# Performance work log

Measured on AMD Instinct MI355X. Metric: run time of the kernel, lower is better.

The kernel has to match this reference:

```python
import jax, jax.numpy as jnp
import numpy as np

V, E, H, L, F, NQ, C = 32000, 256, 8, 4, 1024, 256, 10
B, S = 8, 1024
DK = E // H


def setup_inputs() -> dict:
    key = jax.random.key(0)
    ks = jax.random.split(key, 10)
    f = lambda k, shape, s=0.02: jax.random.normal(k, shape, jnp.float32) * s
    return {
        'tokens': jax.random.randint(ks[0], (B, S), 0, V, jnp.int32),
        'emb': f(ks[1], (V, E), 1.0),
        'theta_attn': f(ks[2], (L, H, DK), 0.5),
        'Wc': f(ks[3], (L, E, E)),
        'bc': jnp.zeros((L, E), jnp.float32),
        'g1': jnp.ones((L, E), jnp.float32),
        'bn1': jnp.zeros((L, E), jnp.float32),
        'theta_ffn': f(ks[4], (L, NQ), 0.5),
        'W1': f(ks[5], (L, NQ, F)),
        'b1': jnp.zeros((L, F), jnp.float32),
        'W2': f(ks[6], (L, F, E)),
        'b2': jnp.zeros((L, E), jnp.float32),
        'g2': jnp.ones((L, E), jnp.float32),
        'bn2': jnp.zeros((L, E), jnp.float32),
        'Wcls': f(ks[7], (E, C)),
        'bcls': jnp.zeros((C,), jnp.float32),
    }


def _ln(x, g, b, eps=1e-5):
    m = x.mean(-1, keepdims=True)
    v = ((x - m) ** 2).mean(-1, keepdims=True)
    return (x - m) / jnp.sqrt(v + eps) * g + b


def _pos_encoding(seq, dim):
    pos = jnp.arange(seq, dtype=jnp.float32)[:, None]
    div = jnp.exp(jnp.arange(0, dim, 2, dtype=jnp.float32) * (-np.log(10000.0) / dim))
    pe = jnp.zeros((seq, dim), jnp.float32)
    pe = pe.at[:, 0::2].set(jnp.sin(pos * div)).at[:, 1::2].set(jnp.cos(pos * div))
    return pe


def _qattn_proj(xh, theta):
    # xh: [B,S,H,dk], theta: [H,dk]. Circuit RX(x+th) per wire, CNOT ring, <Z_i>.
    # Analytic: <Z_i> = prod_{j<=i} cos(phi_j) for i>=1; <Z_0> = prod_{j>=1} cos(phi_j)
    c = jnp.cos(xh + theta)              # [B,S,H,dk]
    cum = jnp.cumprod(c, axis=-1)        # cum[...,i] = prod_{j<=i} c_j
    head0 = jnp.prod(c[..., 1:], axis=-1, keepdims=True)
    return jnp.concatenate([head0, cum[..., 1:]], axis=-1)  # [B,S,H,dk]


def _forward(tokens, emb, theta_attn, Wc, bc, g1, bn1, theta_ffn, W1, b1, W2, b2, g2, bn2, Wcls, bcls):
    b, s = tokens.shape
    x = emb[tokens] + _pos_encoding(s, E)  # [B,S,E]
    scale = 1.0 / np.sqrt(DK)
    for l in range(L):
        # quantum multi-head projection; q = k = v (same deterministic circuit)
        xh = x.reshape(b, s, H, DK)
        p = _qattn_proj(xh, theta_attn[l]).reshape(b, s, E)
        scores = jax.nn.softmax(jnp.einsum('bqe,bke->bqk', p, p) * scale, axis=-1)
        attn = jnp.einsum('bqk,bke->bqe', scores, p) @ Wc[l] + bc[l]
        x = _ln(x + attn, g1[l], bn1[l])
        # quantum FFN: <Z_i> = cos(x_i) * cos(theta_i), NQ == E here
        q = jnp.cos(x[..., :NQ]) * jnp.cos(theta_ffn[l])
        f = jax.nn.relu(q @ W1[l] + b1[l]) @ W2[l] + b2[l]
        x = _ln(x + f, g2[l], bn2[l])
    return x.mean(axis=1) @ Wcls + bcls  # [B,C]


def reference(tokens, emb, theta_attn, Wc, bc, g1, bn1, theta_ffn, W1, b1, W2, b2, g2, bn2, Wcls, bcls):
    return _forward(tokens, emb, theta_attn, Wc, bc, g1, bn1, theta_ffn, W1, b1, W2, b2, g2, bn2, Wcls, bcls)
```

## Files before the change

kernel.cpp:

```cpp
#include <hip/hip_runtime.h>
#include <hip/hip_bf16.h>
#include <math.h>

#define BB 8
#define SS 1024
#define EE 256
#define HH 8
#define DKK 32
#define LL 4
#define FF 1024
#define NQQ 256
#define CC 10

typedef __attribute__((ext_vector_type(8))) short short8;
typedef __attribute__((ext_vector_type(4))) short s16x4;
typedef __attribute__((ext_vector_type(4))) float f32x4;

static __device__ __forceinline__ f32x4 mfma16(short8 a, short8 b, f32x4 c) {
    return __builtin_amdgcn_mfma_f32_16x16x32_bf16(a, b, c, 0, 0, 0);
}
static __device__ __forceinline__ short f2bf(float f) {
    __hip_bfloat16 h = __float2bfloat16(f);
    return *reinterpret_cast<short*>(&h);
}

#define FRAG(P, tile, KG, kg, l) ((P) + (((size_t)((tile)*(KG) + (kg)))*64 + (l))*8)

static __device__ __forceinline__ void qproj_row(
        const float* __restrict__ xrow,
        const float* __restrict__ th,
        int b, int s, int h,
        short* __restrict__ PQ, short* __restrict__ PT) {
    float v[DKK];
    float cum = __cosf(xrow[h * DKK + 0] + th[0]);
    float prod1 = 1.0f;
    #pragma unroll
    for (int j = 1; j < DKK; ++j) {
        float c = __cosf(xrow[h * DKK + j] + th[j]);
        cum *= c;
        prod1 *= c;
        v[j] = cum;
    }
    v[0] = prod1;
    short* pq = PQ + (size_t)b * SS * EE;
    int stile = s >> 4, lr = s & 15;
    #pragma unroll
    for (int lg = 0; lg < 4; ++lg) {
        short8 u;
        #pragma unroll
        for (int j = 0; j < 8; ++j) u[j] = f2bf(v[lg*8 + j]);
        *(short8*)FRAG(pq, stile*8 + h, 1, 0, lg*16 + lr) = u;
    }
    short* pt = PT + (size_t)b * SS * EE;
    int kt = s >> 5, lgs = (s >> 3) & 3, j0 = s & 7;
    #pragma unroll
    for (int j = 0; j < DKK; ++j) {
        int e = h * DKK + j;
        FRAG(pt, e >> 4, 32, kt, lgs*16 + (e & 15))[j0] = f2bf(v[j]);
    }
}

__global__ __launch_bounds__(512) void k_embedq(
        const int* __restrict__ tokens, const float* __restrict__ emb,
        const float* __restrict__ theta_q,
        float* __restrict__ x, short* __restrict__ PQ, short* __restrict__ PT) {
    const int t = threadIdx.x;
    const int tok0 = blockIdx.x * 32;
    __shared__ float xls[32 * 268];
    {
        int r = t >> 4, c0 = (t & 15) * 16;
        int bs = tok0 + r;
        int s  = bs & (SS - 1);
        int tok = tokens[bs];
        const float* er = emb + (size_t)tok * EE + c0;
        float vals[16];
        #pragma unroll
        for (int i = 0; i < 16; ++i) {
            int col = c0 + i;
            int i2 = col >> 1;
            float div = __expf(-(float)(2 * i2) * (logf(10000.0f) / (float)EE));
            float ang = (float)s * div;
            float pe = (col & 1) ? __cosf(ang) : __sinf(ang);
            vals[i] = er[i] + pe;
            xls[r * 268 + col] = vals[i];
        }
        float* xg = x + (size_t)bs * EE + c0;
        #pragma unroll
        for (int i4 = 0; i4 < 4; ++i4)
            *(float4*)(xg + i4 * 4) = *(const float4*)&vals[i4 * 4];
    }
    __syncthreads();
    if (t < 256) {
        int sl = t >> 3, h = t & 7;
        int bs = tok0 + sl;
        qproj_row(&xls[sl * 268], theta_q + h * DKK,
                  bs >> 10, bs & (SS - 1), h, PQ, PT);
    }
}

__global__ __launch_bounds__(256) void k_trall(
        const float* __restrict__ W1, const float* __restrict__ W2,
        const float* __restrict__ Wc,
        short* __restrict__ W1P, short* __restrict__ W2P, short* __restrict__ WcP) {
    int bid = blockIdx.x;
    int lyr = bid / 576, rem = bid % 576;
    const float* in; short* out; int R, C, tile;
    if (rem < 256)      { in = W1 + (size_t)lyr*NQQ*FF; out = W1P + (size_t)lyr*FF*NQQ; R = NQQ; C = FF;  tile = rem; }
    else if (rem < 512) { in = W2 + (size_t)lyr*FF*EE;  out = W2P + (size_t)lyr*EE*FF;  R = FF;  C = EE;  tile = rem - 256; }
    else                { in = Wc + (size_t)lyr*EE*EE;  out = WcP + (size_t)lyr*EE*EE;  R = EE;  C = EE;  tile = rem - 512; }
    const int KG = R >> 5;
    int tiles_c = C >> 5;
    int tc = tile % tiles_c, tr = tile / tiles_c;
    __shared__ float tl[32][33];
    int t = threadIdx.x;
    int rr = t >> 5, cc = t & 31;
    #pragma unroll
    for (int i = 0; i < 4; ++i)
        tl[rr + i*8][cc] = in[(size_t)(tr*32 + rr + i*8) * C + tc*32 + cc];
    __syncthreads();
    int ro = t >> 3, co = (t & 7) * 4;
    int n = tc*32 + ro;
    int k = tr*32 + co;
    int ntile = n >> 4, lr = n & 15;
    int kg = k >> 5, lg = (k & 31) >> 3, j0 = k & 7;
    s16x4 v;
    v[0] = f2bf(tl[co + 0][ro]);
    v[1] = f2bf(tl[co + 1][ro]);
    v[2] = f2bf(tl[co + 2][ro]);
    v[3] = f2bf(tl[co + 3][ro]);
    *(s16x4*)(FRAG(out, ntile, KG, kg, lg*16 + lr) + j0) = v;
}

__global__ __launch_bounds__(256) void k_attn7(const short* __restrict__ PQ,
                                               const short* __restrict__ PT,
                                               short* __restrict__ YP) {
    const int b   = blockIdx.x >> 6;
    const int qt  = blockIdx.x & 63;
    const int tid = threadIdx.x;
    const int w   = tid >> 6;
    const int l   = tid & 63;
    const int lr  = l & 15, lg = l >> 4;
    const short* pq = PQ + (size_t)b * SS * EE;
    const short* pt = PT + (size_t)b * SS * EE;

    __shared__ float accP[2][16][264];
    __shared__ float lsL[4][16];
    __shared__ short wlds[4][16 * 40];

    short8 qf[8];
    #pragma unroll
    for (int kg = 0; kg < 8; ++kg)
        qf[kg] = *(const short8*)FRAG(pq, qt*8 + kg, 1, 0, l);

    f32x4 acc[16];
    #pragma unroll
    for (int i = 0; i < 16; ++i) acc[i] = f32x4{0.f, 0.f, 0.f, 0.f};
    float ls[4] = {0.f, 0.f, 0.f, 0.f};
    const float scale = 0.17677669529663687f;
    short* wl = wlds[w];

    for (int i = 0; i < 8; ++i) {
        const int kt = w + 4 * i;
        short8 sb0[8], sb1[8];
        #pragma unroll
        for (int kg = 0; kg < 8; ++kg) {
            sb0[kg] = *(const short8*)FRAG(pq, (2*kt)*8   + kg, 1, 0, l);
            sb1[kg] = *(const short8*)FRAG(pq, (2*kt+1)*8 + kg, 1, 0, l);
        }
        f32x4 s0a = {0.f,0.f,0.f,0.f}, s0b = {0.f,0.f,0.f,0.f};
        f32x4 s1a = {0.f,0.f,0.f,0.f}, s1b = {0.f,0.f,0.f,0.f};
        #pragma unroll
        for (int kg = 0; kg < 4; ++kg) {
            s0a = mfma16(qf[kg], sb0[kg], s0a);
            s1a = mfma16(qf[kg], sb1[kg], s1a);
        }
        #pragma unroll
        for (int kg = 4; kg < 8; ++kg) {
            s0b = mfma16(qf[kg], sb0[kg], s0b);
            s1b = mfma16(qf[kg], sb1[kg], s1b);
        }
        short8 pvb0[8];
        #pragma unroll
        for (int nt = 0; nt < 8; ++nt)
            pvb0[nt] = *(const short8*)FRAG(pt, nt, 32, kt, l);

        #pragma unroll
        for (int r = 0; r < 4; ++r) {
            float p0 = __expf((s0a[r] + s0b[r]) * scale);
            float p1 = __expf((s1a[r] + s1b[r]) * scale);
            ls[r] += p0 + p1;
            int q = lg * 4 + r;
            wl[q * 40 + lr]      = f2bf(p0);
            wl[q * 40 + 16 + lr] = f2bf(p1);
        }
        short8 pa = *(const short8*)(wl + lr * 40 + lg * 8);
        short8 pvb1[8];
        #pragma unroll
        for (int nt = 0; nt < 8; ++nt)
            pvb1[nt] = *(const short8*)FRAG(pt, 8 + nt, 32, kt, l);
        #pragma unroll
        for (int nt = 0; nt < 8; ++nt)
            acc[nt] = mfma16(pa, pvb0[nt], acc[nt]);
        #pragma unroll
        for (int nt = 0; nt < 8; ++nt)
            acc[8 + nt] = mfma16(pa, pvb1[nt], acc[8 + nt]);
    }

    #pragma unroll
    for (int r = 0; r < 4; ++r) {
        ls[r] += __shfl_xor(ls[r], 1);
        ls[r] += __shfl_xor(ls[r], 2);
        ls[r] += __shfl_xor(ls[r], 4);
        ls[r] += __shfl_xor(ls[r], 8);
    }
    if (lr == 0) {
        #pragma unroll
        for (int r = 0; r < 4; ++r)
            lsL[w][lg * 4 + r] = ls[r];
    }

    if (w >= 2) {
        #pragma unroll
        for (int nt = 0; nt < 16; ++nt)
            #pragma unroll
            for (int r = 0; r < 4; ++r)
                accP[w - 2][lg * 4 + r][nt * 16 + lr] = acc[nt][r];
    }
    __syncthreads();
    if (w < 2) {
        #pragma unroll
        for (int nt = 0; nt < 16; ++nt)
            #pragma unroll
            for (int r = 0; r < 4; ++r)
                accP[w][lg * 4 + r][nt * 16 + lr] += acc[nt][r];
    }
    __syncthreads();

    const int q = tid >> 4, c = tid & 15;
    float L = lsL[0][q] + lsL[1][q] + lsL[2][q] + lsL[3][q];
    float inv = 1.0f / L;
    short ov[16];
    #pragma unroll
    for (int j = 0; j < 4; ++j) {
        float4 a  = *(const float4*)&accP[0][q][c * 16 + j * 4];
        float4 bb = *(const float4*)&accP[1][q][c * 16 + j * 4];
        ov[j*4 + 0] = f2bf((a.x + bb.x) * inv);
        ov[j*4 + 1] = f2bf((a.y + bb.y) * inv);
        ov[j*4 + 2] = f2bf((a.z + bb.z) * inv);
        ov[j*4 + 3] = f2bf((a.w + bb.w) * inv);
    }
    short* yb = YP + (size_t)b * SS * EE;
    int kgo = c >> 1, lgo = (c & 1) * 2;
    *(short8*)FRAG(yb, qt*8 + kgo, 1, 0, lgo*16 + q)     = *(const short8*)&ov[0];
    *(short8*)FRAG(yb, qt*8 + kgo, 1, 0, (lgo+1)*16 + q) = *(const short8*)&ov[8];
}

__global__ __launch_bounds__(512) void k_wcffnq(
        const short* __restrict__ YP, const short* __restrict__ WcP,
        const float* __restrict__ bc, const float* __restrict__ g1,
        const float* __restrict__ bn1,
        const float* __restrict__ tf, const short* __restrict__ W1P,
        const float* __restrict__ b1, const short* __restrict__ W2P,
        const float* __restrict__ b2, const float* __restrict__ g2,
        const float* __restrict__ bn2,
        float* __restrict__ x,
        const float* __restrict__ theta_q, short* __restrict__ PQ,
        short* __restrict__ PT, int has_next) {
    const int t = threadIdx.x, w = t >> 6, l = t & 63;
    const int lr = l & 15, lg = l >> 4;
    const int wg = w >> 2, wn = w & 3;
    const int blk = blockIdx.x;
    const int tok0 = blk * 32;
    const int b = blk >> 5;
    const int qt0 = (blk & 31) * 2;

    __shared__ __align__(16) char smem[34304 + 16384 + 16384];
    float* outw = (float*)smem;
    char*  qls  = smem + 34304;
    char*  hls  = smem + 34304 + 16384;
    float* fout = (float*)(smem + 34304);

    const short* yb = YP + (size_t)b * SS * EE;

    {
        short8 af[8];
        #pragma unroll
        for (int kg = 0; kg < 8; ++kg)
            af[kg] = *(const short8*)FRAG(yb, (qt0 + wg)*8 + kg, 1, 0, l);
        f32x4 acc[4];
        #pragma unroll
        for (int i = 0; i < 4; ++i) acc[i] = f32x4{0.f,0.f,0.f,0.f};
        #pragma unroll
        for (int nt = 0; nt < 4; ++nt) {
            #pragma unroll
            for (int kg = 0; kg < 8; ++kg) {
                short8 bv = *(const short8*)FRAG(WcP, wn*4 + nt, 8, kg, l);
                acc[nt] = mfma16(af[kg], bv, acc[nt]);
            }
        }
        #pragma unroll
        for (int nt = 0; nt < 4; ++nt) {
            int e = wn * 64 + nt * 16 + lr;
            float bce = bc[e];
            #pragma unroll
            for (int r = 0; r < 4; ++r)
                outw[(wg*16 + lg*4 + r) * 268 + e] = acc[nt][r] + bce;
        }
    }
    __syncthreads();

    #pragma unroll
    for (int j = 0; j < 4; ++j) {
        int q = w * 4 + j;
        float4 v  = *(float4*)&outw[q * 268 + l * 4];
        float4 xv = *(const float4*)(x + (size_t)(tok0 + q) * EE + l * 4);
        v.x += xv.x; v.y += xv.y; v.z += xv.z; v.w += xv.w;
        float s = v.x + v.y + v.z + v.w;
        for (int off = 32; off > 0; off >>= 1) s += __shfl_xor(s, off);
        float mean = s * (1.0f / EE);
        float4 d;
        d.x = v.x - mean; d.y = v.y - mean; d.z = v.z - mean; d.w = v.w - mean;
        float s2 = d.x*d.x + d.y*d.y + d.z*d.z + d.w*d.w;
        for (int off = 32; off > 0; off >>= 1) s2 += __shfl_xor(s2, off);
        float inv = rsqrtf(s2 * (1.0f / EE) + 1e-5f);
        float4 gv  = *(const float4*)(g1  + l * 4);
        float4 bnv = *(const float4*)(bn1 + l * 4);
        float4 o;
        o.x = d.x * inv * gv.x + bnv.x;
        o.y = d.y * inv * gv.y + bnv.y;
        o.z = d.z * inv * gv.z + bnv.z;
        o.w = d.w * inv * gv.w + bnv.w;
        *(float4*)&outw[q * 268 + l * 4] = o;
        float4 tv = *(const float4*)(tf + l * 4);
        float q0 = __cosf(o.x) * __cosf(tv.x);
        float q1 = __cosf(o.y) * __cosf(tv.y);
        float q2 = __cosf(o.z) * __cosf(tv.z);
        float q3 = __cosf(o.w) * __cosf(tv.w);
        int byte = (q * 512 + l * 8) ^ ((q & 7) << 4);
        *(unsigned*)(qls + byte) =
            (unsigned)(unsigned short)f2bf(q0) | ((unsigned)(unsigned short)f2bf(q1) << 16);
        *(unsigned*)(qls + byte + 4) =
            (unsigned)(unsigned short)f2bf(q2) | ((unsigned)(unsigned short)f2bf(q3) << 16);
    }
    __syncthreads();

    f32x4 acc2[2][2];
    #pragma unroll
    for (int mt = 0; mt < 2; ++mt)
        #pragma unroll
        for (int nt = 0; nt < 2; ++nt) acc2[mt][nt] = f32x4{0.f,0.f,0.f,0.f};

    for (int fc = 0; fc < 4; ++fc) {
        f32x4 acc1[2][2];
        #pragma unroll
        for (int mt = 0; mt < 2; ++mt)
            #pragma unroll
            for (int i = 0; i < 2; ++i) acc1[mt][i] = f32x4{0.f,0.f,0.f,0.f};
        #pragma unroll
        for (int kg = 0; kg < 8; ++kg) {
            int ca = (kg*32 + lg*8) * 2;
            short8 a0 = *(const short8*)(qls + ((lr*512      + ca) ^ ((lr & 7) << 4)));
            short8 a1 = *(const short8*)(qls + (((16+lr)*512 + ca) ^ ((lr & 7) << 4)));
            #pragma unroll
            for (int i = 0; i < 2; ++i) {
                short8 bv = *(const short8*)FRAG(W1P, fc*16 + w*2 + i, 8, kg, l);
                acc1[0][i] = mfma16(a0, bv, acc1[0][i]);
                acc1[1][i] = mfma16(a1, bv, acc1[1][i]);
            }
        }
        #pragma unroll
        for (int mt = 0; mt < 2; ++mt) {
            #pragma unroll
            for (int i = 0; i < 2; ++i) {
                int fg   = (fc*16 + w*2 + i) * 16 + lr;
                int fcol = (w*2 + i) * 16 + lr;
                float bb = b1[fg];
                #pragma unroll
                for (int r = 0; r < 4; ++r) {
                    int tq = mt * 16 + lg * 4 + r;
                    float hv = fmaxf(acc1[mt][i][r] + bb, 0.0f);
                    int byte = (tq * 512 + fcol * 2) ^ ((tq & 7) << 4);
                    *(short*)(hls + byte) = f2bf(hv);
                }
            }
        }
        __syncthreads();
        #pragma unroll
        for (int k8 = 0; k8 < 8; ++k8) {
            int ca = (k8*32 + lg*8) * 2;
            short8 h0 = *(const short8*)(hls + ((lr*512      + ca) ^ ((lr & 7) << 4)));
            short8 h1 = *(const short8*)(hls + (((16+lr)*512 + ca) ^ ((lr & 7) << 4)));
            #pragma unroll
            for (int nt = 0; nt < 2; ++nt) {
                short8 bv = *(const short8*)FRAG(W2P, w*2 + nt, 32, fc*8 + k8, l);
                acc2[0][nt] = mfma16(h0, bv, acc2[0][nt]);
                acc2[1][nt] = mfma16(h1, bv, acc2[1][nt]);
            }
        }
        __syncthreads();
    }

    #pragma unroll
    for (int mt = 0; mt < 2; ++mt) {
        #pragma unroll
        for (int nt = 0; nt < 2; ++nt) {
            int e = (w*2 + nt) * 16 + lr;
            float b2e = b2[e];
            #pragma unroll
            for (int r = 0; r < 4; ++r)
                fout[(mt*16 + lg*4 + r) * 256 + e] = acc2[mt][nt][r] + b2e;
        }
    }
    __syncthreads();

    #pragma unroll
    for (int j = 0; j < 4; ++j) {
        int q = w * 4 + j;
        float4 v  = *(float4*)&fout[q * 256 + l * 4];
        float4 x1 = *(float4*)&outw[q * 268 + l * 4];
        v.x += x1.x; v.y += x1.y; v.z += x1.z; v.w += x1.w;
        float s = v.x + v.y + v.z + v.w;
        for (int off = 32; off > 0; off >>= 1) s += __shfl_xor(s, off);
        float mean = s * (1.0f / EE);
        float4 d;
        d.x = v.x - mean; d.y = v.y - mean; d.z = v.z - mean; d.w = v.w - mean;
        float s2 = d.x*d.x + d.y*d.y + d.z*d.z + d.w*d.w;
        for (int off = 32; off > 0; off >>= 1) s2 += __shfl_xor(s2, off);
        float inv = rsqrtf(s2 * (1.0f / EE) + 1e-5f);
        float4 gv  = *(const float4*)(g2  + l * 4);
        float4 bnv = *(const float4*)(bn2 + l * 4);
        float4 o;
        o.x = d.x * inv * gv.x + bnv.x;
        o.y = d.y * inv * gv.y + bnv.y;
        o.z = d.z * inv * gv.z + bnv.z;
        o.w = d.w * inv * gv.w + bnv.w;
        *(float4*)(x + (size_t)(tok0 + q) * EE + l * 4) = o;
        *(float4*)&outw[q * 268 + l * 4] = o;
    }
    __syncthreads();

    if (has_next && t < 256) {
        int sl = t >> 3, h = t & 7;
        int bs = tok0 + sl;
        qproj_row(&outw[sl * 268], theta_q + h * DKK,
                  bs >> 10, bs & (SS - 1), h, PQ, PT);
    }
}

__global__ void k_head(const float* __restrict__ x,
                       const float* __restrict__ Wcls,
                       const float* __restrict__ bcls,
                       float* __restrict__ out) {
    int b = blockIdx.x;
    int t = threadIdx.x;
    __shared__ float xm[EE];
    float acc = 0.0f;
    for (int s = 0; s < SS; ++s) acc += x[(size_t)(b * SS + s) * EE + t];
    xm[t] = acc * (1.0f / (float)SS);
    __syncthreads();
    if (t < CC) {
        float a = bcls[t];
        #pragma unroll 8
        for (int e = 0; e < EE; ++e) a += xm[e] * Wcls[e * CC + t];
        out[b * CC + t] = a;
    }
}

extern "C" void kernel_launch(void* const* d_in, const int* in_sizes, int n_in,
                              void* d_out, int out_size, void* d_ws, size_t ws_size,
                              hipStream_t stream) {
    (void)in_sizes; (void)n_in; (void)out_size; (void)ws_size;
    const int*   tokens     = (const int*)d_in[0];
    const float* emb        = (const float*)d_in[1];
    const float* theta_attn = (const float*)d_in[2];
    const float* Wc         = (const float*)d_in[3];
    const float* bc         = (const float*)d_in[4];
    const float* g1         = (const float*)d_in[5];
    const float* bn1        = (const float*)d_in[6];
    const float* theta_ffn  = (const float*)d_in[7];
    const float* W1         = (const float*)d_in[8];
    const float* b1         = (const float*)d_in[9];
    const float* W2         = (const float*)d_in[10];
    const float* b2         = (const float*)d_in[11];
    const float* g2         = (const float*)d_in[12];
    const float* bn2        = (const float*)d_in[13];
    const float* Wcls       = (const float*)d_in[14];
    const float* bcls       = (const float*)d_in[15];
    float* out = (float*)d_out;

    const size_t nTok = (size_t)BB * SS * EE;
    float* x    = (float*)d_ws;
    short* PQ   = (short*)(x + nTok);
    short* PT   = PQ  + nTok;
    short* YP   = PT  + nTok;
    short* W1P  = YP  + nTok;
    short* W2P  = W1P + (size_t)LL * FF * NQQ;
    short* WcP  = W2P + (size_t)LL * EE * FF;

    k_embedq<<<(BB * SS) / 32, 512, 0, stream>>>(tokens, emb, theta_attn, x, PQ, PT);
    k_trall<<<LL * 576, 256, 0, stream>>>(W1, W2, Wc, W1P, W2P, WcP);

    for (int l = 0; l < LL; ++l) {
        int has_next = (l + 1 < LL) ? 1 : 0;
        const float* thq = theta_attn + (size_t)(has_next ? l + 1 : 0) * HH * DKK;
        k_attn7<<<BB * 64, 256, 0, stream>>>(PQ, PT, YP);
        k_wcffnq<<<(BB * SS) / 32, 512, 0, stream>>>(
            YP, WcP + (size_t)l * EE * EE, bc + (size_t)l * EE,
            g1 + (size_t)l * EE, bn1 + (size_t)l * EE,
            theta_ffn + (size_t)l * NQQ,
            W1P + (size_t)l * FF * NQQ, b1 + (size_t)l * FF,
            W2P + (size_t)l * EE * FF, b2 + (size_t)l * EE,
            g2 + (size_t)l * EE, bn2 + (size_t)l * EE,
            x, thq, PQ, PT, has_next);
    }

    k_head<<<BB, 256, 0, stream>>>(x, Wcls, bcls, out);
}
```

Before: 287.7 us.

## Split attention key loop over 8 waves and parallelize mean-pool head

The attention kernel now runs 512 threads per block, so each of 8 waves handles 4 key tiles instead of 8, and partial outputs are reduced through a larger shared-memory buffer. The classifier head is split into a 256-block partial-sum kernel plus a small finishing kernel, replacing 8 blocks that each serially summed 1024 rows. The aim is more parallelism in attention and the head. In exchange it adds shared memory use, a larger cross-wave reduction, and one extra kernel launch.

```diff
diff --git a/kernel.cpp b/kernel.cpp
--- a/kernel.cpp
+++ b/kernel.cpp
@@ -131,7 +131,7 @@
     *(s16x4*)(FRAG(out, ntile, KG, kg, lg*16 + lr) + j0) = v;
 }
 
-__global__ __launch_bounds__(256) void k_attn7(const short* __restrict__ PQ,
+__global__ __launch_bounds__(512) void k_attn8(const short* __restrict__ PQ,
                                                const short* __restrict__ PT,
                                                short* __restrict__ YP) {
     const int b   = blockIdx.x >> 6;
@@ -143,9 +143,9 @@
     const short* pq = PQ + (size_t)b * SS * EE;
     const short* pt = PT + (size_t)b * SS * EE;
 
-    __shared__ float accP[2][16][264];
-    __shared__ float lsL[4][16];
-    __shared__ short wlds[4][16 * 40];
+    __shared__ float accP[4][16][264];
+    __shared__ float lsL[8][16];
+    __shared__ short wlds[8][16 * 40];
 
     short8 qf[8];
     #pragma unroll
@@ -159,8 +159,8 @@
     const float scale = 0.17677669529663687f;
     short* wl = wlds[w];
 
-    for (int i = 0; i < 8; ++i) {
-        const int kt = w + 4 * i;
+    for (int i = 0; i < 4; ++i) {
+        const int kt = w + 8 * i;
         short8 sb0[8], sb1[8];
         #pragma unroll
         for (int kg = 0; kg < 8; ++kg) {
@@ -219,15 +219,15 @@
             lsL[w][lg * 4 + r] = ls[r];
     }
 
-    if (w >= 2) {
+    if (w >= 4) {
         #pragma unroll
         for (int nt = 0; nt < 16; ++nt)
             #pragma unroll
             for (int r = 0; r < 4; ++r)
-                accP[w - 2][lg * 4 + r][nt * 16 + lr] = acc[nt][r];
-    }
-    __syncthreads();
-    if (w < 2) {
+                accP[w - 4][lg * 4 + r][nt * 16 + lr] = acc[nt][r];
+    }
+    __syncthreads();
+    if (w < 4) {
         #pragma unroll
         for (int nt = 0; nt < 16; ++nt)
             #pragma unroll
@@ -236,23 +236,28 @@
     }
     __syncthreads();
 
-    const int q = tid >> 4, c = tid & 15;
-    float L = lsL[0][q] + lsL[1][q] + lsL[2][q] + lsL[3][q];
-    float inv = 1.0f / L;
-    short ov[16];
-    #pragma unroll
-    for (int j = 0; j < 4; ++j) {
-        float4 a  = *(const float4*)&accP[0][q][c * 16 + j * 4];
-        float4 bb = *(const float4*)&accP[1][q][c * 16 + j * 4];
-        ov[j*4 + 0] = f2bf((a.x + bb.x) * inv);
-        ov[j*4 + 1] = f2bf((a.y + bb.y) * inv);
-        ov[j*4 + 2] = f2bf((a.z + bb.z) * inv);
-        ov[j*4 + 3] = f2bf((a.w + bb.w) * inv);
-    }
-    short* yb = YP + (size_t)b * SS * EE;
-    int kgo = c >> 1, lgo = (c & 1) * 2;
-    *(short8*)FRAG(yb, qt*8 + kgo, 1, 0, lgo*16 + q)     = *(const short8*)&ov[0];
-    *(short8*)FRAG(yb, qt*8 + kgo, 1, 0, (lgo+1)*16 + q) = *(const short8*)&ov[8];
+    if (tid < 256) {
+        const int q = tid >> 4, c = tid & 15;
+        float L = lsL[0][q] + lsL[1][q] + lsL[2][q] + lsL[3][q]
+                + lsL[4][q] + lsL[5][q] + lsL[6][q] + lsL[7][q];
+        float inv = 1.0f / L;
+        short ov[16];
+        #pragma unroll
+        for (int j = 0; j < 4; ++j) {
+            float4 a0 = *(const float4*)&accP[0][q][c * 16 + j * 4];
+            float4 a1 = *(const float4*)&accP[1][q][c * 16 + j * 4];
+            float4 a2 = *(const float4*)&accP[2][q][c * 16 + j * 4];
+            float4 a3 = *(const float4*)&accP[3][q][c * 16 + j * 4];
+            ov[j*4 + 0] = f2bf((a0.x + a1.x + a2.x + a3.x) * inv);
+            ov[j*4 + 1] = f2bf((a0.y + a1.y + a2.y + a3.y) * inv);
+            ov[j*4 + 2] = f2bf((a0.z + a1.z + a2.z + a3.z) * inv);
+            ov[j*4 + 3] = f2bf((a0.w + a1.w + a2.w + a3.w) * inv);
+        }
+        short* yb = YP + (size_t)b * SS * EE;
+        int kgo = c >> 1, lgo = (c & 1) * 2;
+        *(short8*)FRAG(yb, qt*8 + kgo, 1, 0, lgo*16 + q)     = *(const short8*)&ov[0];
+        *(short8*)FRAG(yb, qt*8 + kgo, 1, 0, (lgo+1)*16 + q) = *(const short8*)&ov[8];
+    }
 }
 
 __global__ __launch_bounds__(512) void k_wcffnq(
@@ -447,15 +452,29 @@
     }
 }
 
-__global__ void k_head(const float* __restrict__ x,
-                       const float* __restrict__ Wcls,
-                       const float* __restrict__ bcls,
-                       float* __restrict__ out) {
+__global__ __launch_bounds__(256) void k_head1(const float* __restrict__ x,
+                                               float* __restrict__ hpart) {
+    int blk = blockIdx.x;
+    int b = blk >> 5, ch = blk & 31;
+    int t = threadIdx.x;
+    float acc = 0.0f;
+    #pragma unroll 8
+    for (int s = ch * 32; s < ch * 32 + 32; ++s)
+        acc += x[((size_t)b * SS + s) * EE + t];
+    hpart[(size_t)blk * EE + t] = acc;
+}
+
+__global__ __launch_bounds__(256) void k_head2(const float* __restrict__ hpart,
+                                               const float* __restrict__ Wcls,
+                                               const float* __restrict__ bcls,
+                                               float* __restrict__ out) {
     int b = blockIdx.x;
     int t = threadIdx.x;
     __shared__ float xm[EE];
     float acc = 0.0f;
-    for (int s = 0; s < SS; ++s) acc += x[(size_t)(b * SS + s) * EE + t];
+    #pragma unroll 8
+    for (int j = 0; j < 32; ++j)
+        acc += hpart[(size_t)(b * 32 + j) * EE + t];
     xm[t] = acc * (1.0f / (float)SS);
     __syncthreads();
     if (t < CC) {
@@ -489,13 +508,14 @@
     float* out = (float*)d_out;
 
     const size_t nTok = (size_t)BB * SS * EE;
-    float* x    = (float*)d_ws;
-    short* PQ   = (short*)(x + nTok);
-    short* PT   = PQ  + nTok;
-    short* YP   = PT  + nTok;
-    short* W1P  = YP  + nTok;
-    short* W2P  = W1P + (size_t)LL * FF * NQQ;
-    short* WcP  = W2P + (size_t)LL * EE * FF;
+    float* x     = (float*)d_ws;
+    short* PQ    = (short*)(x + nTok);
+    short* PT    = PQ  + nTok;
+    short* YP    = PT  + nTok;
+    short* W1P   = YP  + nTok;
+    short* W2P   = W1P + (size_t)LL * FF * NQQ;
+    short* WcP   = W2P + (size_t)LL * EE * FF;
+    float* hpart = (float*)(WcP + (size_t)LL * EE * EE);
 
     k_embedq<<<(BB * SS) / 32, 512, 0, stream>>>(tokens, emb, theta_attn, x, PQ, PT);
     k_trall<<<LL * 576, 256, 0, stream>>>(W1, W2, Wc, W1P, W2P, WcP);
@@ -503,7 +523,7 @@
     for (int l = 0; l < LL; ++l) {
         int has_next = (l + 1 < LL) ? 1 : 0;
         const float* thq = theta_attn + (size_t)(has_next ? l + 1 : 0) * HH * DKK;
-        k_attn7<<<BB * 64, 256, 0, stream>>>(PQ, PT, YP);
+        k_attn8<<<BB * 64, 512, 0, stream>>>(PQ, PT, YP);
         k_wcffnq<<<(BB * SS) / 32, 512, 0, stream>>>(
             YP, WcP + (size_t)l * EE * EE, bc + (size_t)l * EE,
             g1 + (size_t)l * EE, bn1 + (size_t)l * EE,
@@ -514,5 +534,6 @@
             x, thq, PQ, PT, has_next);
     }
 
-    k_head<<<BB, 256, 0, stream>>>(x, Wcls, bcls, out);
-}
+    k_head1<<<BB * 32, 256, 0, stream>>>(x, hpart);
+    k_head2<<<BB, 256, 0, stream>>>(hpart, Wcls, bcls, out);
+}
```

New measurement: 298.9 us. +3.9%, slower.

## Interleave batch across block IDs and split head mean-pool into two stages

Applied to the files above, without the earlier changes.

Block indices in the embed, attention and FFN kernels are remapped so consecutive blocks cycle through batches. The aim is to spread each batch's work across XCDs and L2 slices. The final head's serial 1024-step mean over 8 blocks becomes a 256-block partial-sum kernel followed by a small reduce-and-classify kernel. This adds one extra launch and a small workspace buffer in exchange for far more parallelism in the tail.

```diff
diff --git a/kernel.cpp b/kernel.cpp
--- a/kernel.cpp
+++ b/kernel.cpp
@@ -65,7 +65,8 @@
         const float* __restrict__ theta_q,
         float* __restrict__ x, short* __restrict__ PQ, short* __restrict__ PT) {
     const int t = threadIdx.x;
-    const int tok0 = blockIdx.x * 32;
+    const int bsw = blockIdx.x & 7, local = blockIdx.x >> 3;
+    const int tok0 = bsw * SS + local * 32;
     __shared__ float xls[32 * 268];
     {
         int r = t >> 4, c0 = (t & 15) * 16;
@@ -134,8 +135,8 @@
 __global__ __launch_bounds__(256) void k_attn7(const short* __restrict__ PQ,
                                                const short* __restrict__ PT,
                                                short* __restrict__ YP) {
-    const int b   = blockIdx.x >> 6;
-    const int qt  = blockIdx.x & 63;
+    const int b   = blockIdx.x & 7;
+    const int qt  = blockIdx.x >> 3;
     const int tid = threadIdx.x;
     const int w   = tid >> 6;
     const int l   = tid & 63;
@@ -269,10 +270,10 @@
     const int t = threadIdx.x, w = t >> 6, l = t & 63;
     const int lr = l & 15, lg = l >> 4;
     const int wg = w >> 2, wn = w & 3;
-    const int blk = blockIdx.x;
-    const int tok0 = blk * 32;
-    const int b = blk >> 5;
-    const int qt0 = (blk & 31) * 2;
+    const int b = blockIdx.x & 7;
+    const int local = blockIdx.x >> 3;
+    const int tok0 = b * SS + local * 32;
+    const int qt0 = local * 2;
 
     __shared__ __align__(16) char smem[34304 + 16384 + 16384];
     float* outw = (float*)smem;
@@ -447,15 +448,28 @@
     }
 }
 
-__global__ void k_head(const float* __restrict__ x,
-                       const float* __restrict__ Wcls,
-                       const float* __restrict__ bcls,
-                       float* __restrict__ out) {
+__global__ __launch_bounds__(256) void k_head1(const float* __restrict__ x,
+                                               float* __restrict__ hpart) {
+    int b = blockIdx.x & 7, ch = blockIdx.x >> 3;
+    int t = threadIdx.x;
+    float acc = 0.0f;
+    #pragma unroll 8
+    for (int s = ch * 32; s < ch * 32 + 32; ++s)
+        acc += x[((size_t)b * SS + s) * EE + t];
+    hpart[(size_t)(b * 32 + ch) * EE + t] = acc;
+}
+
+__global__ __launch_bounds__(256) void k_head2(const float* __restrict__ hpart,
+                                               const float* __restrict__ Wcls,
+                                               const float* __restrict__ bcls,
+                                               float* __restrict__ out) {
     int b = blockIdx.x;
     int t = threadIdx.x;
     __shared__ float xm[EE];
     float acc = 0.0f;
-    for (int s = 0; s < SS; ++s) acc += x[(size_t)(b * SS + s) * EE + t];
+    #pragma unroll 8
+    for (int j = 0; j < 32; ++j)
+        acc += hpart[(size_t)(b * 32 + j) * EE + t];
     xm[t] = acc * (1.0f / (float)SS);
     __syncthreads();
     if (t < CC) {
@@ -489,13 +503,14 @@
     float* out = (float*)d_out;
 
     const size_t nTok = (size_t)BB * SS * EE;
-    float* x    = (float*)d_ws;
-    short* PQ   = (short*)(x + nTok);
-    short* PT   = PQ  + nTok;
-    short* YP   = PT  + nTok;
-    short* W1P  = YP  + nTok;
-    short* W2P  = W1P + (size_t)LL * FF * NQQ;
-    short* WcP  = W2P + (size_t)LL * EE * FF;
+    float* x     = (float*)d_ws;
+    short* PQ    = (short*)(x + nTok);
+    short* PT    = PQ  + nTok;
+    short* YP    = PT  + nTok;
+    short* W1P   = YP  + nTok;
+    short* W2P   = W1P + (size_t)LL * FF * NQQ;
+    short* WcP   = W2P + (size_t)LL * EE * FF;
+    float* hpart = (float*)(WcP + (size_t)LL * EE * EE);
 
     k_embedq<<<(BB * SS) / 32, 512, 0, stream>>>(tokens, emb, theta_attn, x, PQ, PT);
     k_trall<<<LL * 576, 256, 0, stream>>>(W1, W2, Wc, W1P, W2P, WcP);
@@ -514,5 +529,6 @@
             x, thq, PQ, PT, has_next);
     }
 
-    k_head<<<BB, 256, 0, stream>>>(x, Wcls, bcls, out);
-}
+    k_head1<<<BB * 32, 256, 0, stream>>>(x, hpart);
+    k_head2<<<BB, 256, 0, stream>>>(hpart, Wcls, bcls, out);
+}
```

Measured after the change: 248.4 us. 13.7% less time.
